# Optimization experiments

Hardware: AMD Instinct MI355X
Metric: run time of the kernel (lower is better)

The kernel has to match this reference:

```python
import jax, jax.numpy as jnp
import numpy as np

D_IN, D_OUT, SEQ, BATCH = 768, 768, 4096, 4

def setup_inputs() -> dict:
    key = jax.random.key(0)
    k0, k1, k2, k3 = jax.random.split(key, 4)
    s = 1.0 / np.sqrt(D_IN)
    return {
        "input_batch": jax.random.normal(k0, (BATCH, SEQ, D_IN), dtype=jnp.float32),
        "Wq": jax.random.uniform(k1, (D_OUT, D_IN), jnp.float32, -s, s),
        "Wk": jax.random.uniform(k2, (D_OUT, D_IN), jnp.float32, -s, s),
        "Wv": jax.random.uniform(k3, (D_OUT, D_IN), jnp.float32, -s, s),
    }

def reference(input_batch, Wq, Wk, Wv):
    B, N, d_in = input_batch.shape
    q = jnp.einsum('bnd,od->bno', input_batch, Wq)  # [B,N,d_out]
    k = jnp.einsum('bnd,od->bno', input_batch, Wk)
    v = jnp.einsum('bnd,od->bno', input_batch, Wv)
    scores = jnp.einsum('bqo,bko->bqk', q, k)  # [B,N,N]
    causal = jnp.tril(jnp.ones((N, N), dtype=bool))
    scores = jnp.where(causal, scores, -jnp.inf)
    # note: original scales by d_in (input embedding dim), not d_out
    weights = jax.nn.softmax(scores / jnp.sqrt(jnp.asarray(d_in, scores.dtype)), axis=-1)
    return jnp.einsum('bqk,bko->bqo', weights, v)
```

## Files before the change

### kernel.cpp

```cpp
#include <hip/hip_runtime.h>
#include <hip/hip_bf16.h>
#include <stdint.h>

#define NSEQ 4096
#define DDIM 768
#define NB   4
#define NTRI 528
#define BLKE 16384

typedef short short8 __attribute__((ext_vector_type(8)));
typedef float f32x16 __attribute__((ext_vector_type(16)));

__device__ __forceinline__ unsigned short f2bf(float f) {
    unsigned int u = __float_as_uint(f);
    u += 0x7fffu + ((u >> 16) & 1u);
    return (unsigned short)(u >> 16);
}
__device__ __forceinline__ short8 cvt8(const float* __restrict__ p) {
    float4 x = *(const float4*)p;
    float4 y = *(const float4*)(p + 4);
    union { short8 s; __hip_bfloat162 h[4]; } u;
    u.h[0] = __float22bfloat162_rn(make_float2(x.x, x.y));
    u.h[1] = __float22bfloat162_rn(make_float2(x.z, x.w));
    u.h[2] = __float22bfloat162_rn(make_float2(y.x, y.y));
    u.h[3] = __float22bfloat162_rn(make_float2(y.z, y.w));
    return u.s;
}

typedef const __attribute__((address_space(1))) unsigned int ga_u32;
typedef __attribute__((address_space(3))) unsigned int ls_u32;
__device__ __forceinline__ void gload_lds16(const void* g, void* l) {
    __builtin_amdgcn_global_load_lds((ga_u32*)(uintptr_t)g, (ls_u32*)(uintptr_t)l, 16, 0, 0);
}

__device__ __forceinline__ void stage_tile(const unsigned short* gbase, int stride,
                                           unsigned short* lds, int tid) {
    const int lane = tid & 63, wv = tid >> 6;
    const int r8  = lane >> 3;
    const int cl  = (lane & 7) * 8;
#pragma unroll
    for (int t = 0; t < 4; ++t) {
        const int row = wv * 32 + t * 8 + r8;
        const int csw = (((lane & 7) ^ r8 ^ t) & 7) * 8;
        gload_lds16(gbase + (size_t)row * stride + csw, lds + row * 64 + cl);
    }
}

__device__ __forceinline__ void stage_tile8(const unsigned short* gbase, int stride,
                                            unsigned short* lds, int tid) {
    const int lane = tid & 63, wv = tid >> 6;
    const int r8  = lane >> 3;
    const int cl  = (lane & 7) * 8;
    const int rb  = wv * 8 + r8;
    const int csw = (((lane & 7) ^ r8 ^ (wv & 3)) & 7) * 8;
#pragma unroll
    for (int s = 0; s < 4; ++s) {
        const int row = s * 64 + rb;
        gload_lds16(gbase + (size_t)row * stride + csw, lds + row * 64 + cl);
    }
}

__device__ __forceinline__ void mma_tiles(const unsigned short* As, const unsigned short* Bs,
                                          f32x16 acc[2][2], int wm, int wn, int lane) {
    const int r32 = lane & 31;
    const int hi  = lane >> 5;
    const int sw  = (lane & 7) ^ ((lane >> 3) & 3);
#pragma unroll
    for (int c = 0; c < 4; ++c) {
        const int chunk = (((c * 2 + hi) ^ sw) & 7) * 8;
        short8 af[2], bg[2];
#pragma unroll
        for (int mt = 0; mt < 2; ++mt)
            af[mt] = *(const short8*)(As + (wm * 64 + mt * 32 + r32) * 64 + chunk);
#pragma unroll
        for (int nt = 0; nt < 2; ++nt)
            bg[nt] = *(const short8*)(Bs + (wn * 64 + nt * 32 + r32) * 64 + chunk);
#pragma unroll
        for (int mt = 0; mt < 2; ++mt)
#pragma unroll
            for (int nt = 0; nt < 2; ++nt)
                acc[mt][nt] = __builtin_amdgcn_mfma_f32_32x32x16_bf16(af[mt], bg[nt], acc[mt][nt], 0, 0, 0);
    }
}

__device__ __forceinline__ int crow(int reg, int hi) {
    return (reg & 3) + 8 * (reg >> 2) + 4 * hi;
}

__device__ __forceinline__ void group_compute(
    const unsigned short* __restrict__ Asb, const unsigned short* __restrict__ Bsb,
    const unsigned short* a_src, const unsigned short* b_src, int stride,
    unsigned short* a_dst, unsigned short* b_dst, bool do_stage,
    f32x16 (&acc)[4][2], int wm, int wn, int lane, int tid)
{
    const int r32 = lane & 31, hi = lane >> 5;
    const int sw  = (lane & 7) ^ ((lane >> 3) & 3);

    if (do_stage) {
        stage_tile8(a_src, stride, a_dst, tid);
        stage_tile8(b_src, stride, b_dst, tid);
    }

    short8 bg[2][4];
    const unsigned short* Bw = Bsb + (size_t)(wn * 64 + r32) * 64;
#pragma unroll
    for (int c = 0; c < 4; ++c) {
        const int chunk = (((c * 2 + hi) ^ sw) & 7) * 8;
        bg[0][c] = *(const short8*)(Bw + chunk);
        bg[1][c] = *(const short8*)(Bw + 32 * 64 + chunk);
    }

#pragma unroll
    for (int mt = 0; mt < 4; ++mt) {
        short8 af[4];
        const unsigned short* Aw = Asb + (size_t)(wm * 128 + mt * 32 + r32) * 64;
#pragma unroll
        for (int c = 0; c < 4; ++c)
            af[c] = *(const short8*)(Aw + (((c * 2 + hi) ^ sw) & 7) * 8);
        __builtin_amdgcn_s_barrier();
        asm volatile("s_waitcnt lgkmcnt(0)" ::: "memory");
        __builtin_amdgcn_sched_barrier(0);
        __builtin_amdgcn_s_setprio(1);
#pragma unroll
        for (int c = 0; c < 4; ++c) {
            acc[mt][0] = __builtin_amdgcn_mfma_f32_32x32x16_bf16(af[c], bg[0][c], acc[mt][0], 0, 0, 0);
            acc[mt][1] = __builtin_amdgcn_mfma_f32_32x32x16_bf16(af[c], bg[1][c], acc[mt][1], 0, 0, 0);
        }
        __builtin_amdgcn_s_setprio(0);
    }
    asm volatile("s_waitcnt vmcnt(0)" ::: "memory");
    __builtin_amdgcn_s_barrier();
}

__global__ __launch_bounds__(256)
void convert_kernel(const float* __restrict__ X, const float* __restrict__ Wq,
                    const float* __restrict__ Wk, const float* __restrict__ Wv,
                    unsigned short* __restrict__ Xb, unsigned short* __restrict__ Wb,
                    float* __restrict__ L, unsigned int* __restrict__ counter)
{
    const int bid = blockIdx.x;
    if (bid == 0 && threadIdx.x == 0) *counter = 0u;
    if (bid >= 7008) {
        const int idx = (bid - 7008) * 1024 + threadIdx.x * 4;
        *(float4*)(L + idx) = make_float4(0.f, 0.f, 0.f, 0.f);
        return;
    }
    const float* src; unsigned short* dst; size_t off;
    if (bid < 6144) { src = X; dst = Xb; off = (size_t)bid * 2048; }
    else {
        const int wbid = bid - 6144;
        const int wi = wbid / 288;
        src = (wi == 0) ? Wq : ((wi == 1) ? Wk : Wv);
        dst = Wb + (size_t)wi * (DDIM * DDIM);
        off = (size_t)(wbid - wi * 288) * 2048;
    }
    const size_t i = off + (size_t)threadIdx.x * 8;
    *(short8*)(dst + i) = cvt8(src + i);
}

__global__ __launch_bounds__(512, 2)
void qkv_gemm(const unsigned short* __restrict__ Xb, const unsigned short* __restrict__ Wb,
              unsigned short* __restrict__ Qb, unsigned short* __restrict__ Kb,
              unsigned short* __restrict__ Vtb)
{
    const int tid = threadIdx.x, lane = tid & 63, wv = tid >> 6;
    const int r32 = lane & 31, hi = lane >> 5, wm = wv >> 2, wn = wv & 3;
    const int m0 = blockIdx.x * 256, n0 = blockIdx.y * 256, widx = blockIdx.z;
    const unsigned short* A = Xb + (size_t)m0 * DDIM;
    const unsigned short* B = Wb + (size_t)widx * (DDIM * DDIM) + (size_t)n0 * DDIM;

    __shared__ __align__(16) unsigned short As[2][256 * 64];
    __shared__ __align__(16) unsigned short Bs[2][256 * 64];

    f32x16 acc[4][2] = {};

    stage_tile8(A, DDIM, As[0], tid);
    stage_tile8(B, DDIM, Bs[0], tid);
    asm volatile("s_waitcnt vmcnt(0)" ::: "memory");
    __builtin_amdgcn_s_barrier();

    for (int t = 0; t < 12; ++t) {
        const int p = t & 1;
        group_compute(As[p], Bs[p],
                      A + (t + 1) * 64, B + (t + 1) * 64, DDIM,
                      As[1 - p], Bs[1 - p], t + 1 < 12,
                      acc, wm, wn, lane, tid);
    }

    const int m_base = m0 + wm * 128, o_base = n0 + wn * 64;
    if (widx < 2) {
        unsigned short* dst = (widx == 0) ? Qb : Kb;
#pragma unroll
        for (int mt = 0; mt < 4; ++mt)
#pragma unroll
            for (int nt = 0; nt < 2; ++nt)
#pragma unroll
                for (int reg = 0; reg < 16; ++reg)
                    dst[(size_t)(m_base + mt * 32 + crow(reg, hi)) * DDIM +
                        (o_base + nt * 32 + r32)] = f2bf(acc[mt][nt][reg]);
    } else {
        const int bb = m0 >> 12;
        const int n_seq0 = (m0 & (NSEQ - 1)) + wm * 128;
#pragma unroll
        for (int mt = 0; mt < 4; ++mt)
#pragma unroll
            for (int nt = 0; nt < 2; ++nt) {
                const int o = o_base + nt * 32 + r32;
#pragma unroll
                for (int b4 = 0; b4 < 4; ++b4) {
                    ushort4 pk;
                    pk.x = f2bf(acc[mt][nt][b4 * 4 + 0]);
                    pk.y = f2bf(acc[mt][nt][b4 * 4 + 1]);
                    pk.z = f2bf(acc[mt][nt][b4 * 4 + 2]);
                    pk.w = f2bf(acc[mt][nt][b4 * 4 + 3]);
                    const int n = n_seq0 + mt * 32 + b4 * 8 + hi * 4;
                    *(ushort4*)(Vtb + ((size_t)(bb * DDIM + o)) * NSEQ + n) = pk;
                }
            }
    }
}

__global__ __launch_bounds__(512, 2)
void gemm_s(const unsigned short* __restrict__ Qb, const unsigned short* __restrict__ Kb,
            unsigned short* __restrict__ Sbuf, float* __restrict__ L)
{
    const float c2 = 0.05205877475f;
    const int tid = threadIdx.x, lane = tid & 63, wv = tid >> 6;
    const int r32 = lane & 31, hi = lane >> 5, wm = wv >> 2, wn = wv & 3;
    const int idx = blockIdx.x, bb = blockIdx.y;
    int qsb = (int)((sqrtf(8.f * idx + 1.f) - 1.f) * 0.5f);
    while ((qsb + 1) * (qsb + 2) / 2 <= idx) ++qsb;
    while (qsb * (qsb + 1) / 2 > idx) --qsb;
    const int ksb = idx - qsb * (qsb + 1) / 2;

    const unsigned short* A = Qb + ((size_t)bb * NSEQ + qsb * 256) * DDIM;
    const unsigned short* B = Kb + ((size_t)bb * NSEQ + ksb * 256) * DDIM;

    __shared__ __align__(16) unsigned short As[2][256 * 64];
    __shared__ __align__(16) unsigned short Bs[2][256 * 64];

    f32x16 acc[4][2] = {};

    stage_tile8(A, DDIM, As[0], tid);
    stage_tile8(B, DDIM, Bs[0], tid);
    asm volatile("s_waitcnt vmcnt(0)" ::: "memory");
    __builtin_amdgcn_s_barrier();

    for (int t = 0; t < 12; ++t) {
        const int p = t & 1;
        group_compute(As[p], Bs[p],
                      A + (t + 1) * 64, B + (t + 1) * 64, DDIM,
                      As[1 - p], Bs[1 - p], t + 1 < 12,
                      acc, wm, wn, lane, tid);
    }

    const int qb128 = qsb * 2 + wm;
    const int kb128 = ksb * 2 + (wn >> 1);
    if (kb128 > qb128) return;
    unsigned short* Sblk = Sbuf + ((size_t)(bb * NTRI + qb128 * (qb128 + 1) / 2 + kb128)) * BLKE;
    float* Lrow = L + (size_t)bb * NSEQ + (qb128 << 7);
    const int coff = (wn & 1) * 64;
    const bool diag = (qb128 == kb128);
#pragma unroll
    for (int mt = 0; mt < 4; ++mt)
#pragma unroll
        for (int rp = 0; rp < 8; ++rp) {
            const int reg0 = rp * 2, reg1 = reg0 + 1;
            const int row0 = mt * 32 + crow(reg0, hi);
            const int row1 = row0 + 1;
            float vs0 = 0.f, vs1 = 0.f;
#pragma unroll
            for (int nt = 0; nt < 2; ++nt) {
                const int col = coff + nt * 32 + r32;
                float e0 = (diag && col > row0) ? 0.f : exp2f(acc[mt][nt][reg0] * c2);
                float e1 = (diag && col > row1) ? 0.f : exp2f(acc[mt][nt][reg1] * c2);
                union { __hip_bfloat162 h; ushort2 u; } cv;
                cv.h = __float22bfloat162_rn(make_float2(e0, e1));
                Sblk[row0 * 128 + col] = cv.u.x;
                Sblk[row1 * 128 + col] = cv.u.y;
                vs0 += e0;
                vs1 += e1;
            }
#pragma unroll
            for (int s = 1; s < 32; s <<= 1) {
                vs0 += __shfl_xor(vs0, s);
                vs1 += __shfl_xor(vs1, s);
            }
            if (r32 == 0) {
                atomicAdd(&Lrow[row0], vs0);
                atomicAdd(&Lrow[row1], vs1);
            }
        }
}

__global__ __launch_bounds__(256)
void gemm_pv(const unsigned short* __restrict__ P, const unsigned short* __restrict__ Vt,
             const float* __restrict__ L, float* __restrict__ Out,
             unsigned int* __restrict__ counter)
{
    const int tid = threadIdx.x, lane = tid & 63, wv = tid >> 6;
    const int r32 = lane & 31, hi = lane >> 5, wm = wv >> 1, wn = wv & 1;

    __shared__ __align__(16) unsigned short As[128 * 64];
    __shared__ __align__(16) unsigned short Bs[128 * 64];
    __shared__ float Linv[128];
    __shared__ unsigned int item_s;

    for (;;) {
        if (tid == 0) item_s = atomicAdd(counter, 1u);
        __syncthreads();
        const unsigned int item = item_s;
        if (item >= 768u) return;

        const int t = (int)(item / 24u);
        const int qb = 31 - t;
        const int rem = (int)(item - (unsigned)t * 24u);
        const int bb = rem / 6, ob = rem % 6;
        const size_t triq = (size_t)qb * (qb + 1) / 2;
        const unsigned short* Pbat = P + (size_t)bb * NTRI * BLKE;
        const unsigned short* Bbase = Vt + ((size_t)(bb * DDIM + ob * 128)) * NSEQ;
        const int niter = (qb + 1) * 2;

        if (tid < 128) Linv[tid] = 1.0f / L[(size_t)bb * NSEQ + qb * 128 + tid];

        f32x16 acc[2][2] = {};

        for (int it = 0; it < niter; ++it) {
            const int k0 = it * 64;
            const int kblk = k0 >> 7, cb = k0 & 64;
            stage_tile(Pbat + (triq + kblk) * BLKE + cb, 128, As, tid);
            stage_tile(Bbase + k0, NSEQ, Bs, tid);
            __syncthreads();
            mma_tiles(As, Bs, acc, wm, wn, lane);
            __syncthreads();
        }

        const int o_base = ob * 128 + wn * 64;
#pragma unroll
        for (int mt = 0; mt < 2; ++mt)
#pragma unroll
            for (int nt = 0; nt < 2; ++nt)
#pragma unroll
                for (int reg = 0; reg < 16; ++reg) {
                    const int rl = wm * 64 + mt * 32 + crow(reg, hi);
                    const int q = qb * 128 + rl;
                    Out[((size_t)(bb * NSEQ + q)) * DDIM + (o_base + nt * 32 + r32)] =
                        acc[mt][nt][reg] * Linv[rl];
                }
    }
}

extern "C" void kernel_launch(void* const* d_in, const int* in_sizes, int n_in,
                              void* d_out, int out_size, void* d_ws, size_t ws_size,
                              hipStream_t stream)
{
    const float* X  = (const float*)d_in[0];
    const float* Wq = (const float*)d_in[1];
    const float* Wk = (const float*)d_in[2];
    const float* Wv = (const float*)d_in[3];
    float* Out = (float*)d_out;

    const size_t E = (size_t)NB * NSEQ * DDIM;
    char* ws = (char*)d_ws;
    unsigned short* Qb  = (unsigned short*)ws;
    unsigned short* Kb  = Qb + E;
    unsigned short* Vtb = Kb + E;
    unsigned short* Sbuf = Vtb + E;
    unsigned short* Xb  = Sbuf;
    unsigned short* Wb  = Xb + E;
    float* L = (float*)(ws + 3 * E * 2 + (size_t)NB * NTRI * BLKE * 2);
    unsigned int* counter = (unsigned int*)(L + (size_t)NB * NSEQ);

    convert_kernel<<<7024, 256, 0, stream>>>(X, Wq, Wk, Wv, Xb, Wb, L, counter);
    qkv_gemm<<<dim3(64, 3, 3), 512, 0, stream>>>(Xb, Wb, Qb, Kb, Vtb);
    gemm_s<<<dim3(136, NB), 512, 0, stream>>>(Qb, Kb, Sbuf, L);
    gemm_pv<<<512, 256, 0, stream>>>(Sbuf, Vtb, L, Out, counter);
}
```

Baseline: 376.9 us.

## Pipeline GEMM staging at k16 slice granularity with deep vmcnt prefetch

```diff
diff --git a/kernel.cpp b/kernel.cpp
--- a/kernel.cpp
+++ b/kernel.cpp
@@ -46,20 +46,6 @@
     }
 }
 
-__device__ __forceinline__ void stage_tile8(const unsigned short* gbase, int stride,
-                                            unsigned short* lds, int tid) {
-    const int lane = tid & 63, wv = tid >> 6;
-    const int r8  = lane >> 3;
-    const int cl  = (lane & 7) * 8;
-    const int rb  = wv * 8 + r8;
-    const int csw = (((lane & 7) ^ r8 ^ (wv & 3)) & 7) * 8;
-#pragma unroll
-    for (int s = 0; s < 4; ++s) {
-        const int row = s * 64 + rb;
-        gload_lds16(gbase + (size_t)row * stride + csw, lds + row * 64 + cl);
-    }
-}
-
 __device__ __forceinline__ void mma_tiles(const unsigned short* As, const unsigned short* Bs,
                                           f32x16 acc[2][2], int wm, int wn, int lane) {
     const int r32 = lane & 31;
@@ -87,49 +73,57 @@
     return (reg & 3) + 8 * (reg >> 2) + 4 * hi;
 }
 
-__device__ __forceinline__ void group_compute(
-    const unsigned short* __restrict__ Asb, const unsigned short* __restrict__ Bsb,
-    const unsigned short* a_src, const unsigned short* b_src, int stride,
-    unsigned short* a_dst, unsigned short* b_dst, bool do_stage,
-    f32x16 (&acc)[4][2], int wm, int wn, int lane, int tid)
-{
-    const int r32 = lane & 31, hi = lane >> 5;
-    const int sw  = (lane & 7) ^ ((lane >> 3) & 3);
-
-    if (do_stage) {
-        stage_tile8(a_src, stride, a_dst, tid);
-        stage_tile8(b_src, stride, b_dst, tid);
-    }
-
-    short8 bg[2][4];
-    const unsigned short* Bw = Bsb + (size_t)(wn * 64 + r32) * 64;
-#pragma unroll
-    for (int c = 0; c < 4; ++c) {
-        const int chunk = (((c * 2 + hi) ^ sw) & 7) * 8;
-        bg[0][c] = *(const short8*)(Bw + chunk);
-        bg[1][c] = *(const short8*)(Bw + 32 * 64 + chunk);
-    }
-
-#pragma unroll
-    for (int mt = 0; mt < 4; ++mt) {
-        short8 af[4];
-        const unsigned short* Aw = Asb + (size_t)(wm * 128 + mt * 32 + r32) * 64;
-#pragma unroll
-        for (int c = 0; c < 4; ++c)
-            af[c] = *(const short8*)(Aw + (((c * 2 + hi) ^ sw) & 7) * 8);
-        __builtin_amdgcn_s_barrier();
-        asm volatile("s_waitcnt lgkmcnt(0)" ::: "memory");
-        __builtin_amdgcn_sched_barrier(0);
-        __builtin_amdgcn_s_setprio(1);
+__device__ __forceinline__ void stage_slice(const unsigned short* __restrict__ A,
+                                            const unsigned short* __restrict__ B,
+                                            unsigned short* AsB, unsigned short* BsB,
+                                            int tid, int e) {
+    const int t4 = e >> 2;
+    const int te = (t4 < 12) ? t4 : 11;
+    const int ce = e & 3;
+    const int buf = t4 & 1;
+    const int so = (buf * 4 + ce) * 4096 + tid * 8;
+    const size_t goff = (size_t)(tid >> 1) * DDIM + te * 64 + ce * 16 + (tid & 1) * 8;
+    gload_lds16(A + goff, AsB + so);
+    gload_lds16(B + goff, BsB + so);
+}
+
+__device__ __forceinline__ void gemm256_core(const unsigned short* __restrict__ A,
+                                             const unsigned short* __restrict__ B,
+                                             unsigned short* AsB, unsigned short* BsB,
+                                             f32x16 (&acc)[4][2], int tid) {
+    const int lane = tid & 63, r32 = lane & 31, hi = lane >> 5;
+    const int wv = tid >> 6, wm = wv >> 2, wn = wv & 3;
+#pragma unroll
+    for (int e = 0; e < 7; ++e) stage_slice(A, B, AsB, BsB, tid, e);
+
+    for (int t = 0; t < 12; ++t) {
+        const int buf = t & 1;
 #pragma unroll
         for (int c = 0; c < 4; ++c) {
-            acc[mt][0] = __builtin_amdgcn_mfma_f32_32x32x16_bf16(af[c], bg[0][c], acc[mt][0], 0, 0, 0);
-            acc[mt][1] = __builtin_amdgcn_mfma_f32_32x32x16_bf16(af[c], bg[1][c], acc[mt][1], 0, 0, 0);
+            asm volatile("s_waitcnt vmcnt(12)" ::: "memory");
+            __builtin_amdgcn_s_barrier();
+            __builtin_amdgcn_sched_barrier(0);
+            stage_slice(A, B, AsB, BsB, tid, 4 * t + c + 7);
+            const unsigned short* Asl = AsB + (buf * 4 + c) * 4096;
+            const unsigned short* Bsl = BsB + (buf * 4 + c) * 4096;
+            short8 af[4], bg[2];
+#pragma unroll
+            for (int mt = 0; mt < 4; ++mt)
+                af[mt] = *(const short8*)(Asl + (wm * 128 + mt * 32 + r32) * 16 + hi * 8);
+#pragma unroll
+            for (int nt = 0; nt < 2; ++nt)
+                bg[nt] = *(const short8*)(Bsl + (wn * 64 + nt * 32 + r32) * 16 + hi * 8);
+            asm volatile("s_waitcnt lgkmcnt(0)" ::: "memory");
+            __builtin_amdgcn_sched_barrier(0);
+            __builtin_amdgcn_s_setprio(1);
+#pragma unroll
+            for (int mt = 0; mt < 4; ++mt) {
+                acc[mt][0] = __builtin_amdgcn_mfma_f32_32x32x16_bf16(af[mt], bg[0], acc[mt][0], 0, 0, 0);
+                acc[mt][1] = __builtin_amdgcn_mfma_f32_32x32x16_bf16(af[mt], bg[1], acc[mt][1], 0, 0, 0);
+            }
+            __builtin_amdgcn_s_setprio(0);
         }
-        __builtin_amdgcn_s_setprio(0);
-    }
-    asm volatile("s_waitcnt vmcnt(0)" ::: "memory");
-    __builtin_amdgcn_s_barrier();
+    }
 }
 
 __global__ __launch_bounds__(256)
@@ -169,23 +163,11 @@
     const unsigned short* A = Xb + (size_t)m0 * DDIM;
     const unsigned short* B = Wb + (size_t)widx * (DDIM * DDIM) + (size_t)n0 * DDIM;
 
-    __shared__ __align__(16) unsigned short As[2][256 * 64];
-    __shared__ __align__(16) unsigned short Bs[2][256 * 64];
+    __shared__ __align__(16) unsigned short As[2 * 4 * 4096];
+    __shared__ __align__(16) unsigned short Bs[2 * 4 * 4096];
 
     f32x16 acc[4][2] = {};
-
-    stage_tile8(A, DDIM, As[0], tid);
-    stage_tile8(B, DDIM, Bs[0], tid);
-    asm volatile("s_waitcnt vmcnt(0)" ::: "memory");
-    __builtin_amdgcn_s_barrier();
-
-    for (int t = 0; t < 12; ++t) {
-        const int p = t & 1;
-        group_compute(As[p], Bs[p],
-                      A + (t + 1) * 64, B + (t + 1) * 64, DDIM,
-                      As[1 - p], Bs[1 - p], t + 1 < 12,
-                      acc, wm, wn, lane, tid);
-    }
+    gemm256_core(A, B, As, Bs, acc, tid);
 
     const int m_base = m0 + wm * 128, o_base = n0 + wn * 64;
     if (widx < 2) {
@@ -236,23 +218,11 @@
     const unsigned short* A = Qb + ((size_t)bb * NSEQ + qsb * 256) * DDIM;
     const unsigned short* B = Kb + ((size_t)bb * NSEQ + ksb * 256) * DDIM;
 
-    __shared__ __align__(16) unsigned short As[2][256 * 64];
-    __shared__ __align__(16) unsigned short Bs[2][256 * 64];
+    __shared__ __align__(16) unsigned short As[2 * 4 * 4096];
+    __shared__ __align__(16) unsigned short Bs[2 * 4 * 4096];
 
     f32x16 acc[4][2] = {};
-
-    stage_tile8(A, DDIM, As[0], tid);
-    stage_tile8(B, DDIM, Bs[0], tid);
-    asm volatile("s_waitcnt vmcnt(0)" ::: "memory");
-    __builtin_amdgcn_s_barrier();
-
-    for (int t = 0; t < 12; ++t) {
-        const int p = t & 1;
-        group_compute(As[p], Bs[p],
-                      A + (t + 1) * 64, B + (t + 1) * 64, DDIM,
-                      As[1 - p], Bs[1 - p], t + 1 < 12,
-                      acc, wm, wn, lane, tid);
-    }
+    gemm256_core(A, B, As, Bs, acc, tid);
 
     const int qb128 = qsb * 2 + wm;
     const int kb128 = ksb * 2 + (wn >> 1);
```

After: 415.1 us. +10.1%, slower.
